# Performance work log

Measured on AMD Instinct MI355X. Metric: run time of the kernel, lower is better.

Reference implementation:

```python
import jax, jax.numpy as jnp
import numpy as np

MAX_LORAS, OUT, IN = 8, 4096, 4096
B, S = 4, 2048


def setup_inputs() -> dict:
    key = jax.random.key(0)
    k1, k2, k3 = jax.random.split(key, 3)
    x = jax.random.normal(k1, (B, S, IN), dtype=jnp.float32)
    weight = jax.random.normal(k2, (MAX_LORAS, OUT, IN), dtype=jnp.float32) * 0.02
    adapter_ids = jax.random.randint(k3, (B,), 0, MAX_LORAS, dtype=jnp.int32)
    return {"x": x, "weight": weight, "adapter_ids": adapter_ids}


def reference(x, weight, adapter_ids):
    # Gather a full [OUT, IN] matrix per batch element (matches weight[adapter_ids]).
    w = weight[adapter_ids]                 # [B, OUT, IN]
    # F.linear(x, w) == x @ w^T, batched over B: [B, S, IN] x [B, OUT, IN] -> [B, S, OUT]
    return jnp.einsum('bsi,boi->bso', x, w)
```

## Files before the change

kernel.cpp:

```cpp
#include <hip/hip_runtime.h>
#include <hip/hip_bf16.h>


#define SEQ    2048
#define IN_K   4096
#define OUT_N  4096
#define NB     4

typedef __attribute__((ext_vector_type(8))) short  short8;
typedef __attribute__((ext_vector_type(4))) float  float4v;

constexpr int BM = 256, BN = 256, BK = 32;
constexpr int GT = 512;
constexpr int KTILES = IN_K / BK;

__device__ inline short f2b(float f) {
    union { float f; unsigned u; } v; v.f = f;
    unsigned r = v.u + 0x7FFFu + ((v.u >> 16) & 1u);
    return (short)(r >> 16);
}
__device__ inline short8 pack8(float4v lo, float4v hi) {
    short8 r;
    r[0] = f2b(lo[0]); r[1] = f2b(lo[1]); r[2] = f2b(lo[2]); r[3] = f2b(lo[3]);
    r[4] = f2b(hi[0]); r[5] = f2b(hi[1]); r[6] = f2b(hi[2]); r[7] = f2b(hi[3]);
    return r;
}

typedef const __attribute__((address_space(1))) void* gp1_t;
typedef __attribute__((address_space(3))) void*       lp3_t;
__device__ inline void gload_lds16(const void* g, void* l) {
    __builtin_amdgcn_global_load_lds((gp1_t)g, (lp3_t)l, 16, 0, 0);
}

#define WAITV(N)  asm volatile("s_waitcnt vmcnt(" #N ")" ::: "memory")

__global__ __launch_bounds__(256)
void cvt_x_kernel(const float* __restrict__ x, short* __restrict__ o, int n8)
{
    int i = blockIdx.x * blockDim.x + threadIdx.x;
    const int stride = gridDim.x * blockDim.x;
    for (; i < n8; i += stride) {
        const float4v a = *(const float4v*)(x + (size_t)i * 8);
        const float4v b = *(const float4v*)(x + (size_t)i * 8 + 4);
        *(short8*)(o + (size_t)i * 8) = pack8(a, b);
    }
}

__global__ __launch_bounds__(256)
void cvt_w_kernel(const float* __restrict__ w, const int* __restrict__ ids,
                  short* __restrict__ o, int by_id)
{
    const int b  = blockIdx.y;
    const int id = ids[b];
    int slot = b;
    if (by_id) {
        for (int j = 0; j < b; ++j) if (ids[j] == id) return;
        slot = id;
    }
    const float* __restrict__ src = w + (size_t)id   * OUT_N * IN_K;
    short* __restrict__       dst = o + (size_t)slot * OUT_N * IN_K;
    const int n8 = OUT_N * IN_K / 8;
    int i = blockIdx.x * blockDim.x + threadIdx.x;
    const int stride = gridDim.x * blockDim.x;
    for (; i < n8; i += stride) {
        const float4v a = *(const float4v*)(src + (size_t)i * 8);
        const float4v c = *(const float4v*)(src + (size_t)i * 8 + 4);
        *(short8*)(dst + (size_t)i * 8) = pack8(a, c);
    }
}

__global__ __launch_bounds__(GT, 2)
void mll_gemm_v6(const short* __restrict__ A, const short* __restrict__ W,
                 const int* __restrict__ ids, int by_id, float* __restrict__ out)
{
    __shared__ __align__(16) short lds[4][2 * BM * BK];

    const int tid  = threadIdx.x;
    const int lane = tid & 63;
    const int wid  = tid >> 6;
    const int wr   = wid >> 2;
    const int wc   = wid & 3;

    const int bid = blockIdx.x;
    const int xcd = bid & 7;
    const int i_  = bid >> 3;
    const int rr_ = i_ >> 5;
    const int j_  = i_ & 31;
    const int bz  = xcd >> 1;
    const int bx  = (xcd & 1) * 8 + rr_ * 4 + (j_ >> 3);
    const int by  = j_ & 7;
    const int brow = by * BM, bcol = bx * BN;

    const int wslot = by_id ? ids[bz] : bz;
    const short* __restrict__ Ab = A + (size_t)bz * SEQ * IN_K + (size_t)brow * IN_K;
    const short* __restrict__ Bb = W + (size_t)wslot * OUT_N * IN_K + (size_t)bcol * IN_K;

    const int c0 = tid, c1 = tid + GT;
    const int r0_ = c0 >> 2, s0_ = (c0 & 3) ^ ((r0_ >> 1) & 3);
    const int r1_ = c1 >> 2, s1_ = (c1 & 3) ^ ((r1_ >> 1) & 3);
    const short* pa0 = Ab + (size_t)r0_ * IN_K + s0_ * 8;
    const short* pa1 = Ab + (size_t)r1_ * IN_K + s1_ * 8;
    const short* pb0 = Bb + (size_t)r0_ * IN_K + s0_ * 8;
    const short* pb1 = Bb + (size_t)r1_ * IN_K + s1_ * 8;

    float4v acc[8][4];
#pragma unroll
    for (int m = 0; m < 8; ++m)
#pragma unroll
        for (int q = 0; q < 4; ++q)
            acc[m][q] = (float4v){0.f, 0.f, 0.f, 0.f};

    const int lr  = lane & 15;
    const int ksl = lane >> 4;
    const int ks2 = (ksl ^ ((lr >> 1) & 3)) * 8;

    short8 af[8], bf[4];

#pragma unroll
    for (int tt = 0; tt < 3; ++tt) {
        short* s = &lds[tt][0];
        gload_lds16(pa0 + tt * BK, s + c0 * 8);
        gload_lds16(pa1 + tt * BK, s + c1 * 8);
        gload_lds16(pb0 + tt * BK, s + BM * BK + c0 * 8);
        gload_lds16(pb1 + tt * BK, s + BM * BK + c1 * 8);
    }
    WAITV(8);
    __builtin_amdgcn_s_barrier();

    {
        const short* sA = &lds[0][0];
        const short* sB = sA + BM * BK;
#pragma unroll
        for (int m = 0; m < 8; ++m)
            af[m] = *(const short8*)(sA + (wr * 128 + m * 16 + lr) * BK + ks2);
#pragma unroll
        for (int q = 0; q < 4; ++q)
            bf[q] = *(const short8*)(sB + (wc * 64 + q * 16 + lr) * BK + ks2);
    }

    for (int t = 0; t < KTILES; ++t) {
        if (t + 3 < KTILES) {
            short* d = &lds[(t + 3) & 3][0];
            gload_lds16(pa0 + (t + 3) * BK, d + c0 * 8);
            gload_lds16(pa1 + (t + 3) * BK, d + c1 * 8);
            gload_lds16(pb0 + (t + 3) * BK, d + BM * BK + c0 * 8);
            gload_lds16(pb1 + (t + 3) * BK, d + BM * BK + c1 * 8);
        }

        __builtin_amdgcn_s_setprio(1);
#pragma unroll
        for (int m = 0; m < 8; ++m)
#pragma unroll
            for (int q = 0; q < 4; ++q)
                acc[m][q] = __builtin_amdgcn_mfma_f32_16x16x32_bf16(
                    af[m], bf[q], acc[m][q], 0, 0, 0);
        __builtin_amdgcn_s_setprio(0);

        if (t <= KTILES - 4)      WAITV(8);
        else if (t == KTILES - 3) WAITV(4);
        else if (t == KTILES - 2) WAITV(0);
        __builtin_amdgcn_s_barrier();

        if (t + 1 < KTILES) {
            const short* sA = &lds[(t + 1) & 3][0];
            const short* sB = sA + BM * BK;
#pragma unroll
            for (int m = 0; m < 8; ++m)
                af[m] = *(const short8*)(sA + (wr * 128 + m * 16 + lr) * BK + ks2);
#pragma unroll
            for (int q = 0; q < 4; ++q)
                bf[q] = *(const short8*)(sB + (wc * 64 + q * 16 + lr) * BK + ks2);
        }
    }

    float* __restrict__ ob = out + (size_t)bz * SEQ * OUT_N;
    const int lrow = ksl * 4;
#pragma unroll
    for (int m = 0; m < 8; ++m) {
#pragma unroll
        for (int q = 0; q < 4; ++q) {
            const int r0 = brow + wr * 128 + m * 16 + lrow;
            const int c  = bcol + wc * 64 + q * 16 + lr;
#pragma unroll
            for (int j = 0; j < 4; ++j)
                ob[(size_t)(r0 + j) * OUT_N + c] = acc[m][q][j];
        }
    }
}

__device__ inline int xr(int row) { return (row & 3) ^ ((row >> 2) & 3); }

__global__ __launch_bounds__(256, 2)
void mll_gemm_fused(const float* __restrict__ x,
                    const float* __restrict__ w,
                    const int*   __restrict__ adapter_ids,
                    float* __restrict__ out)
{
    constexpr int FBM = 128, FBN = 128, FBK = 32;
    __shared__ __align__(16) short As[2][FBM * FBK];
    __shared__ __align__(16) short Bs[2][FBN * FBK];

    const int tid  = threadIdx.x;
    const int lane = tid & 63;
    const int wave = tid >> 6;
    const int wr   = wave >> 1;
    const int wc   = wave & 1;

    const int b    = blockIdx.z;
    const int aid  = adapter_ids[b];
    const int brow = blockIdx.y * FBM;
    const int bcol = blockIdx.x * FBN;

    const float* __restrict__ xb = x + (size_t)b   * SEQ   * IN_K;
    const float* __restrict__ wb = w + (size_t)aid * OUT_N * IN_K;

    float4v ra[2][2], rb[2][2];

    auto LOADG = [&](int kt) {
        const int k0 = kt * FBK;
#pragma unroll
        for (int g = 0; g < 2; ++g) {
            const int f  = tid + g * 256;
            const int r  = f >> 2;
            const int sl = f & 3;
            const float* pa = xb + (size_t)(brow + r) * IN_K + k0 + sl * 8;
            ra[g][0] = *(const float4v*)pa;
            ra[g][1] = *(const float4v*)(pa + 4);
            const float* pb = wb + (size_t)(bcol + r) * IN_K + k0 + sl * 8;
            rb[g][0] = *(const float4v*)pb;
            rb[g][1] = *(const float4v*)(pb + 4);
        }
    };
    auto STORE_LDS = [&](int buf) {
#pragma unroll
        for (int g = 0; g < 2; ++g) {
            const int f  = tid + g * 256;
            const int r  = f >> 2;
            const int sl = f & 3;
            const int ss = sl ^ xr(r);
            *(short8*)&As[buf][r * FBK + ss * 8] = pack8(ra[g][0], ra[g][1]);
            *(short8*)&Bs[buf][r * FBK + ss * 8] = pack8(rb[g][0], rb[g][1]);
        }
    };

    float4v acc[4][4];
#pragma unroll
    for (int m = 0; m < 4; ++m)
#pragma unroll
        for (int q = 0; q < 4; ++q)
            acc[m][q] = (float4v){0.f, 0.f, 0.f, 0.f};

    const int NT = IN_K / FBK;
    LOADG(0); STORE_LDS(0); __syncthreads();
    int cur = 0;
    for (int kt = 0; kt < NT; ++kt) {
        if (kt + 1 < NT) LOADG(kt + 1);
        short8 af[4], bfr[4];
        const int ksl = lane >> 4;
#pragma unroll
        for (int m = 0; m < 4; ++m) {
            const int rrk = wr * 64 + m * 16 + (lane & 15);
            af[m] = *(const short8*)&As[cur][rrk * FBK + (ksl ^ xr(rrk)) * 8];
        }
#pragma unroll
        for (int q = 0; q < 4; ++q) {
            const int rc = wc * 64 + q * 16 + (lane & 15);
            bfr[q] = *(const short8*)&Bs[cur][rc * FBK + (ksl ^ xr(rc)) * 8];
        }
#pragma unroll
        for (int m = 0; m < 4; ++m)
#pragma unroll
            for (int q = 0; q < 4; ++q)
                acc[m][q] = __builtin_amdgcn_mfma_f32_16x16x32_bf16(
                    af[m], bfr[q], acc[m][q], 0, 0, 0);
        if (kt + 1 < NT) STORE_LDS(cur ^ 1);
        __syncthreads();
        cur ^= 1;
    }

    float* __restrict__ ob = out + (size_t)b * SEQ * OUT_N;
    const int lrow = (lane >> 4) * 4;
    const int lcol = lane & 15;
#pragma unroll
    for (int m = 0; m < 4; ++m) {
#pragma unroll
        for (int q = 0; q < 4; ++q) {
            const int r0 = brow + wr * 64 + m * 16 + lrow;
            const int c  = bcol + wc * 64 + q * 16 + lcol;
#pragma unroll
            for (int j = 0; j < 4; ++j)
                ob[(size_t)(r0 + j) * OUT_N + c] = acc[m][q][j];
        }
    }
}

extern "C" void kernel_launch(void* const* d_in, const int* in_sizes, int n_in,
                              void* d_out, int out_size, void* d_ws, size_t ws_size,
                              hipStream_t stream)
{
    const float* x   = (const float*)d_in[0];
    const float* w   = (const float*)d_in[1];
    const int*   ids = (const int*)d_in[2];
    float* out = (float*)d_out;

    const size_t xb_bytes   = (size_t)NB * SEQ   * IN_K * sizeof(short);
    const size_t wb4_bytes  = (size_t)NB * OUT_N * IN_K * sizeof(short);
    const size_t wb8_bytes  = (size_t)8  * OUT_N * IN_K * sizeof(short);

    if (ws_size >= xb_bytes + wb8_bytes) {
        short* xb16 = (short*)d_ws;
        short* wb16 = (short*)((char*)d_ws + xb_bytes);
        cvt_x_kernel<<<2048, 256, 0, stream>>>(x, xb16, NB * SEQ * IN_K / 8);
        cvt_w_kernel<<<dim3(1024, NB), 256, 0, stream>>>(w, ids, wb16, 1);
        mll_gemm_v6<<<512, GT, 0, stream>>>(xb16, wb16, ids, 1, out);
    } else if (ws_size >= xb_bytes + wb4_bytes) {
        short* xb16 = (short*)d_ws;
        short* wb16 = (short*)((char*)d_ws + xb_bytes);
        cvt_x_kernel<<<2048, 256, 0, stream>>>(x, xb16, NB * SEQ * IN_K / 8);
        cvt_w_kernel<<<dim3(1024, NB), 256, 0, stream>>>(w, ids, wb16, 0);
        mll_gemm_v6<<<512, GT, 0, stream>>>(xb16, wb16, ids, 0, out);
    } else {
        mll_gemm_fused<<<dim3(OUT_N / 128, SEQ / 128, NB), 256, 0, stream>>>(
            x, w, ids, out);
    }
}
```

Measured before the change: 348.0 us.

## Double BK to 64 with split A/B LDS buffers and staggered prefetch

Doubles the K tile to 64, halving the number of barriers per output tile. The single 4-stage LDS ring is replaced by a 3-stage A buffer and a 2-stage B buffer. Each tile's MFMA work is split into two half-steps so the second half's fragments load from LDS while the first half computes, and A/B global prefetches are issued at different points in the loop. The XOR swizzle becomes 8-way for the wider rows, and the block-to-XCD mapping is simplified. In exchange, the shallower B pipeline exposes more global latency, and the extra fragment registers may hurt occupancy.

```diff
diff --git a/kernel.cpp b/kernel.cpp
--- a/kernel.cpp
+++ b/kernel.cpp
@@ -10,9 +10,9 @@
 typedef __attribute__((ext_vector_type(8))) short  short8;
 typedef __attribute__((ext_vector_type(4))) float  float4v;
 
-constexpr int BM = 256, BN = 256, BK = 32;
+constexpr int BM = 256, BN = 256, BK = 64;
 constexpr int GT = 512;
-constexpr int KTILES = IN_K / BK;
+constexpr int KT = IN_K / BK;
 
 __device__ inline short f2b(float f) {
     union { float f; unsigned u; } v; v.f = f;
@@ -70,10 +70,11 @@
 }
 
 __global__ __launch_bounds__(GT, 2)
-void mll_gemm_v6(const short* __restrict__ A, const short* __restrict__ W,
+void mll_gemm_v9(const short* __restrict__ A, const short* __restrict__ W,
                  const int* __restrict__ ids, int by_id, float* __restrict__ out)
 {
-    __shared__ __align__(16) short lds[4][2 * BM * BK];
+    __shared__ __align__(16) short ldsA[3][BM * BK];
+    __shared__ __align__(16) short ldsB[2][BN * BK];
 
     const int tid  = threadIdx.x;
     const int lane = tid & 63;
@@ -82,26 +83,28 @@
     const int wc   = wid & 3;
 
     const int bid = blockIdx.x;
-    const int xcd = bid & 7;
-    const int i_  = bid >> 3;
-    const int rr_ = i_ >> 5;
-    const int j_  = i_ & 31;
-    const int bz  = xcd >> 1;
-    const int bx  = (xcd & 1) * 8 + rr_ * 4 + (j_ >> 3);
-    const int by  = j_ & 7;
+    const int n   = (bid & 7) * 64 + (bid >> 3);
+    const int bx  = n & 15;
+    const int by  = (n >> 4) & 7;
+    const int bz  = n >> 7;
     const int brow = by * BM, bcol = bx * BN;
 
     const int wslot = by_id ? ids[bz] : bz;
     const short* __restrict__ Ab = A + (size_t)bz * SEQ * IN_K + (size_t)brow * IN_K;
     const short* __restrict__ Bb = W + (size_t)wslot * OUT_N * IN_K + (size_t)bcol * IN_K;
 
-    const int c0 = tid, c1 = tid + GT;
-    const int r0_ = c0 >> 2, s0_ = (c0 & 3) ^ ((r0_ >> 1) & 3);
-    const int r1_ = c1 >> 2, s1_ = (c1 & 3) ^ ((r1_ >> 1) & 3);
-    const short* pa0 = Ab + (size_t)r0_ * IN_K + s0_ * 8;
-    const short* pa1 = Ab + (size_t)r1_ * IN_K + s1_ * 8;
-    const short* pb0 = Bb + (size_t)r0_ * IN_K + s0_ * 8;
-    const short* pb1 = Bb + (size_t)r1_ * IN_K + s1_ * 8;
+    int          offs[4];
+    const short* pA[4];
+    const short* pB[4];
+#pragma unroll
+    for (int k = 0; k < 4; ++k) {
+        const int c   = tid + k * GT;
+        const int row = c >> 3;
+        const int sg  = (c & 7) ^ (row & 7);
+        offs[k] = c * 8;
+        pA[k] = Ab + (size_t)row * IN_K + sg * 8;
+        pB[k] = Bb + (size_t)row * IN_K + sg * 8;
+    }
 
     float4v acc[8][4];
 #pragma unroll
@@ -112,40 +115,43 @@
 
     const int lr  = lane & 15;
     const int ksl = lane >> 4;
-    const int ks2 = (ksl ^ ((lr >> 1) & 3)) * 8;
-
-    short8 af[8], bf[4];
-
-#pragma unroll
-    for (int tt = 0; tt < 3; ++tt) {
-        short* s = &lds[tt][0];
-        gload_lds16(pa0 + tt * BK, s + c0 * 8);
-        gload_lds16(pa1 + tt * BK, s + c1 * 8);
-        gload_lds16(pb0 + tt * BK, s + BM * BK + c0 * 8);
-        gload_lds16(pb1 + tt * BK, s + BM * BK + c1 * 8);
-    }
-    WAITV(8);
+    const int sw  = lr & 7;
+    const int o0  = ((0 + ksl) ^ sw) * 8;
+    const int o1  = ((4 + ksl) ^ sw) * 8;
+
+    const int baseA = (wr * 128 + lr) * BK;
+    const int baseB = (wc * 64  + lr) * BK;
+
+    short8 fA0[8], fA1[8], fB0[4], fB1[4];
+
+#pragma unroll
+    for (int k = 0; k < 4; ++k) gload_lds16(pA[k],          &ldsA[0][offs[k]]);
+#pragma unroll
+    for (int k = 0; k < 4; ++k) gload_lds16(pB[k],          &ldsB[0][offs[k]]);
+#pragma unroll
+    for (int k = 0; k < 4; ++k) gload_lds16(pA[k] + BK,     &ldsA[1][offs[k]]);
+#pragma unroll
+    for (int k = 0; k < 4; ++k) gload_lds16(pB[k] + BK,     &ldsB[1][offs[k]]);
+#pragma unroll
+    for (int k = 0; k < 4; ++k) gload_lds16(pA[k] + 2 * BK, &ldsA[2][offs[k]]);
+    WAITV(12);
     __builtin_amdgcn_s_barrier();
 
     {
-        const short* sA = &lds[0][0];
-        const short* sB = sA + BM * BK;
+        const short* sAp = &ldsA[0][0];
+        const short* sBp = &ldsB[0][0];
 #pragma unroll
         for (int m = 0; m < 8; ++m)
-            af[m] = *(const short8*)(sA + (wr * 128 + m * 16 + lr) * BK + ks2);
+            fA0[m] = *(const short8*)(sAp + baseA + m * 16 * BK + o0);
 #pragma unroll
         for (int q = 0; q < 4; ++q)
-            bf[q] = *(const short8*)(sB + (wc * 64 + q * 16 + lr) * BK + ks2);
-    }
-
-    for (int t = 0; t < KTILES; ++t) {
-        if (t + 3 < KTILES) {
-            short* d = &lds[(t + 3) & 3][0];
-            gload_lds16(pa0 + (t + 3) * BK, d + c0 * 8);
-            gload_lds16(pa1 + (t + 3) * BK, d + c1 * 8);
-            gload_lds16(pb0 + (t + 3) * BK, d + BM * BK + c0 * 8);
-            gload_lds16(pb1 + (t + 3) * BK, d + BM * BK + c1 * 8);
-        }
+            fB0[q] = *(const short8*)(sBp + baseB + q * 16 * BK + o0);
+    }
+
+    int sa = 0;
+    for (int t = 0; t < KT; ++t) {
+        const short* sAp = &ldsA[sa][0];
+        const short* sBp = &ldsB[t & 1][0];
 
         __builtin_amdgcn_s_setprio(1);
 #pragma unroll
@@ -153,23 +159,51 @@
 #pragma unroll
             for (int q = 0; q < 4; ++q)
                 acc[m][q] = __builtin_amdgcn_mfma_f32_16x16x32_bf16(
-                    af[m], bf[q], acc[m][q], 0, 0, 0);
+                    fA0[m], fB0[q], acc[m][q], 0, 0, 0);
         __builtin_amdgcn_s_setprio(0);
-
-        if (t <= KTILES - 4)      WAITV(8);
-        else if (t == KTILES - 3) WAITV(4);
-        else if (t == KTILES - 2) WAITV(0);
-        __builtin_amdgcn_s_barrier();
-
-        if (t + 1 < KTILES) {
-            const short* sA = &lds[(t + 1) & 3][0];
-            const short* sB = sA + BM * BK;
+#pragma unroll
+        for (int m = 0; m < 8; ++m)
+            fA1[m] = *(const short8*)(sAp + baseA + m * 16 * BK + o1);
+#pragma unroll
+        for (int q = 0; q < 4; ++q)
+            fB1[q] = *(const short8*)(sBp + baseB + q * 16 * BK + o1);
+        if (t >= 1 && t + 1 < KT) {
+            short* d = &ldsB[(t + 1) & 1][0];
+#pragma unroll
+            for (int k = 0; k < 4; ++k)
+                gload_lds16(pB[k] + (t + 1) * BK, d + offs[k]);
+        }
+
+        __builtin_amdgcn_s_setprio(1);
+#pragma unroll
+        for (int m = 0; m < 8; ++m)
+#pragma unroll
+            for (int q = 0; q < 4; ++q)
+                acc[m][q] = __builtin_amdgcn_mfma_f32_16x16x32_bf16(
+                    fA1[m], fB1[q], acc[m][q], 0, 0, 0);
+        __builtin_amdgcn_s_setprio(0);
+        int sa2 = sa + 2; if (sa2 >= 3) sa2 -= 3;
+        if (t >= 1 && t + 2 < KT) {
+            short* d = &ldsA[sa2][0];
+#pragma unroll
+            for (int k = 0; k < 4; ++k)
+                gload_lds16(pA[k] + (t + 2) * BK, d + offs[k]);
+        }
+
+        if (t <= KT - 3)      WAITV(4);
+        else if (t == KT - 2) WAITV(0);
+        if (t < KT - 1) {
+            __builtin_amdgcn_s_barrier();
+            int sn = sa + 1; if (sn >= 3) sn -= 3;
+            const short* nA = &ldsA[sn][0];
+            const short* nB = &ldsB[(t + 1) & 1][0];
 #pragma unroll
             for (int m = 0; m < 8; ++m)
-                af[m] = *(const short8*)(sA + (wr * 128 + m * 16 + lr) * BK + ks2);
+                fA0[m] = *(const short8*)(nA + baseA + m * 16 * BK + o0);
 #pragma unroll
             for (int q = 0; q < 4; ++q)
-                bf[q] = *(const short8*)(sB + (wc * 64 + q * 16 + lr) * BK + ks2);
+                fB0[q] = *(const short8*)(nB + baseB + q * 16 * BK + o0);
+            sa = sn;
         }
     }
 
@@ -303,22 +337,22 @@
     const int*   ids = (const int*)d_in[2];
     float* out = (float*)d_out;
 
-    const size_t xb_bytes   = (size_t)NB * SEQ   * IN_K * sizeof(short);
-    const size_t wb4_bytes  = (size_t)NB * OUT_N * IN_K * sizeof(short);
-    const size_t wb8_bytes  = (size_t)8  * OUT_N * IN_K * sizeof(short);
+    const size_t xb_bytes  = (size_t)NB * SEQ   * IN_K * sizeof(short);
+    const size_t wb4_bytes = (size_t)NB * OUT_N * IN_K * sizeof(short);
+    const size_t wb8_bytes = (size_t)8  * OUT_N * IN_K * sizeof(short);
 
     if (ws_size >= xb_bytes + wb8_bytes) {
         short* xb16 = (short*)d_ws;
         short* wb16 = (short*)((char*)d_ws + xb_bytes);
         cvt_x_kernel<<<2048, 256, 0, stream>>>(x, xb16, NB * SEQ * IN_K / 8);
         cvt_w_kernel<<<dim3(1024, NB), 256, 0, stream>>>(w, ids, wb16, 1);
-        mll_gemm_v6<<<512, GT, 0, stream>>>(xb16, wb16, ids, 1, out);
+        mll_gemm_v9<<<512, GT, 0, stream>>>(xb16, wb16, ids, 1, out);
     } else if (ws_size >= xb_bytes + wb4_bytes) {
         short* xb16 = (short*)d_ws;
         short* wb16 = (short*)((char*)d_ws + xb_bytes);
         cvt_x_kernel<<<2048, 256, 0, stream>>>(x, xb16, NB * SEQ * IN_K / 8);
         cvt_w_kernel<<<dim3(1024, NB), 256, 0, stream>>>(w, ids, wb16, 0);
-        mll_gemm_v6<<<512, GT, 0, stream>>>(xb16, wb16, ids, 0, out);
+        mll_gemm_v9<<<512, GT, 0, stream>>>(xb16, wb16, ids, 0, out);
     } else {
         mll_gemm_fused<<<dim3(OUT_N / 128, SEQ / 128, NB), 256, 0, stream>>>(
             x, w, ids, out);
```

Measured after the change: 336.8 us. 3.2% less time.
